# Optimization experiments

Measured on AMD Instinct MI355X. Metric: run time of the kernel, lower is better.

Reference implementation:

```python
import jax, jax.numpy as jnp
import numpy as np

C_IN = 4
C_OUT = 8
K = 5            # kernel_size (hardcoded by reshape(25,2) in original)
N_ROT = 8
R_B = 8          # rot_basis_size
STRIDE = 1
PAD = 2
TWO_PI = 2.0 * np.pi
ROT_SCALE = TWO_PI / R_B


def B2(x):
    # quadratic B-spline, exactly as in the torch source
    return (-3 * (-0.5 + x) ** 2 * jnp.sign(0.5 - x)
            + (-1.5 + x) ** 2 * jnp.sign(1.5 - x)
            - 3 * (1 + 2 * x) ** 2 * jnp.sign(0.5 + x) / 4
            + (3 + 2 * x) ** 2 * jnp.sign(1.5 + x) / 4) / 4


def angle_dist(th1, th2):
    return jnp.mod(th2 - th1 + np.pi, TWO_PI) - np.pi


def make_kernel_stack(weights):
    # weights: (C_IN, R_B*K*K, C_OUT). M = K*K*R_B combined (spatial-center, rot-center) index;
    # original repeats each spatial center R_B times (np.repeat) and tiles rot centers K*K times.
    lidx = -(K // 2)
    coords = jnp.arange(lidx, K // 2 + 1, dtype=jnp.float32)
    grid = jnp.stack(jnp.meshgrid(coords, coords, indexing='ij'), axis=-1)  # (K,K,2), grid[i,j]=[i+l, j+l]
    centers_xy = jnp.repeat(grid.reshape(K * K, 2), R_B, axis=0)            # (M,2)
    rot_centers = jnp.tile(jnp.arange(R_B, dtype=jnp.float32) * ROT_SCALE, K * K)  # (M,)
    rot_sample = jnp.arange(N_ROT, dtype=jnp.float32) * (TWO_PI / N_ROT)    # (N_ROT,)

    def one_kernel(theta):
        c, s = jnp.cos(theta), jnp.sin(theta)
        x, y = grid[..., 0], grid[..., 1]
        xxs = jnp.stack([x * c - y * s, x * s + y * c], axis=-1)            # (K,K,2) rotated sample grid
        xx_diffs = centers_xy[None, None, :, :] - xxs[:, :, None, :]        # (K,K,M,2)
        xx_vals = jnp.prod(B2(xx_diffs), axis=-1)                           # (K,K,M) separable spatial spline
        rots = rot_sample + theta                                           # (N_ROT,)
        rot_vals = B2(angle_dist(rots[:, None], rot_centers[None, :]) / ROT_SCALE)  # (N_ROT,M)
        vals = xx_vals[:, :, None, :] * rot_vals[None, None, :, :]          # (K,K,N_ROT,M)
        # contract basis index m against weights -> (C_OUT, C_IN, N_ROT, K, K)
        return jnp.einsum('xyrm,imo->oirxy', vals, weights)

    ks = jax.vmap(one_kernel)(-rot_sample)  # (N_ROT, C_OUT, C_IN, N_ROT, K, K), matches torch.cat over -theta
    return ks.reshape(N_ROT * C_OUT, C_IN * N_ROT, K, K)


def setup_inputs() -> dict:
    key = jax.random.key(0)
    kx, kw = jax.random.split(key)
    X = jax.random.normal(kx, (8, C_IN, N_ROT, 256, 256), dtype=jnp.float32)
    weights = jax.random.normal(kw, (C_IN, R_B * K * K, C_OUT), dtype=jnp.float32)
    return {'X': X, 'weights': weights}


def reference(X, weights):
    ks = make_kernel_stack(weights)                       # (N_ROT*C_OUT, C_IN*N_ROT, K, K)
    B, c, d, H, W = X.shape
    Xr = X.reshape(B, c * d, H, W)
    out = jax.lax.conv_general_dilated(
        Xr, ks, window_strides=(STRIDE, STRIDE),
        padding=[(PAD, PAD), (PAD, PAD)],
        dimension_numbers=('NCHW', 'OIHW', 'NCHW'))        # (B, N_ROT*C_OUT, h, w)
    Bn, _, h, w = out.shape
    out = out.reshape(Bn, N_ROT, C_OUT, h, w).transpose(0, 2, 1, 3, 4)  # (B, C_OUT, N_ROT, h, w)
    return (TWO_PI / N_ROT) * out
```

## Files before the change

### kernel.cpp

```cpp
#include <hip/hip_runtime.h>
#include <hip/hip_fp16.h>
#include <math.h>

#define PI_F      3.14159265358979323846f
#define TWO_PI_F  6.28318530717958647692f
#define PI4_F     0.78539816339744830962f

typedef _Float16 f16x8 __attribute__((ext_vector_type(8)));
typedef float    f32x4 __attribute__((ext_vector_type(4)));

__device__ __forceinline__ float sgn(float t) {
    return (t > 0.f) ? 1.f : ((t < 0.f) ? -1.f : 0.f);
}

__device__ __forceinline__ float b2(float x) {
    float a = x - 0.5f;
    float b = x - 1.5f;
    float c = 1.f + 2.f * x;
    float d = 3.f + 2.f * x;
    return (-3.f * a * a * sgn(0.5f - x)
            + b * b * sgn(1.5f - x)
            - 0.75f * c * c * sgn(0.5f + x)
            + 0.25f * d * d * sgn(1.5f + x)) * 0.25f;
}

__global__ void build_ks_kernel(const float* __restrict__ w, __half* __restrict__ ksh) {
    int g = blockIdx.x * 256 + threadIdx.x;
    if (g >= 64 * 32 * 25) return;
    int O = g & 63;
    int rest = g >> 6;
    int t = rest % 25;
    int I = rest / 25;
    int r0 = O >> 3, o = O & 7;
    int i = I >> 3, r = I & 7;
    int x = t / 5, y = t % 5;

    float theta = -(float)r0 * PI4_F;
    float cth = cosf(theta), sth = sinf(theta);
    float fx = (float)(x - 2), fy = (float)(y - 2);
    float xc = fx * cth - fy * sth;
    float yc = fx * sth + fy * cth;

    float rotv[8];
    float rs = (float)r * PI4_F + theta;
    #pragma unroll
    for (int mr = 0; mr < 8; ++mr) {
        float v = (float)mr * PI4_F - rs + PI_F;
        float md = fmodf(v, TWO_PI_F);
        if (md < 0.f) md += TWO_PI_F;
        rotv[mr] = b2((md - PI_F) / PI4_F);
    }

    float sum = 0.f;
    for (int mx = 0; mx < 25; ++mx) {
        float cx = (float)(mx / 5 - 2);
        float cy = (float)(mx % 5 - 2);
        float bx = b2(cx - xc) * b2(cy - yc);
        if (bx != 0.f) {
            const float* wp = w + (size_t)(i * 200 + mx * 8) * 8 + o;
            #pragma unroll
            for (int mr = 0; mr < 8; ++mr)
                sum = fmaf(bx * rotv[mr], wp[mr * 8], sum);
        }
    }
    ksh[(size_t)(t * 64 + O) * 32 + I] = __float2half(sum);
}

__global__ __launch_bounds__(256, 3) void conv_fused_kernel(const float* __restrict__ X,
                                                            const __half* __restrict__ ksh,
                                                            float* __restrict__ out) {
    __shared__ uint4 xt[4 * 433];

    int bid = blockIdx.x;
    int b   = bid >> 8;
    int rem = bid & 255;
    int h0  = (rem >> 3) << 3;
    int w0  = (rem & 7) << 5;
    int tid = threadIdx.x;

    const float* Xb = X + (size_t)b * 32 * 65536;

    for (int lin = tid; lin < 1728; lin += 256) {
        int slot = lin / 432;
        int p    = lin - slot * 432;
        int r = p / 36, c = p - (p / 36) * 36;
        int gh = h0 + r - 2;
        int gw = w0 + c - 2;
        union { __half hh[8]; uint4 u; } q;
        if ((unsigned)gh < 256u && (unsigned)gw < 256u) {
            const float* src = Xb + (size_t)slot * 8 * 65536 + gh * 256 + gw;
            #pragma unroll
            for (int j = 0; j < 8; ++j) q.hh[j] = __float2half(src[j * 65536]);
        } else {
            q.u = make_uint4(0u, 0u, 0u, 0u);
        }
        xt[slot * 433 + p] = q.u;
    }
    __syncthreads();

    int wave = tid >> 6, lane = tid & 63;
    int lO = lane & 15, ks4 = lane >> 4;
    int bidx = lO * 4 + ks4;
    const uint4* ksq = (const uint4*)ksh;

    f32x4 acc[4][4] = {};
    int baseA[4];
    #pragma unroll
    for (int m = 0; m < 4; ++m)
        baseA[m] = 433 * ks4 + (wave * 2 + (m >> 1)) * 36 + (m & 1) * 16 + lO;

    f16x8 Bf[2][4];
    #pragma unroll
    for (int n = 0; n < 4; ++n)
        Bf[0][n] = __builtin_bit_cast(f16x8, ksq[n * 64 + bidx]);

    #pragma unroll
    for (int t = 0; t < 25; ++t) {
        const int cur = t & 1, nxt = cur ^ 1;
        const int aoff = (t / 5) * 36 + (t % 5);

        f16x8 Af[4];
        #pragma unroll
        for (int m = 0; m < 4; ++m)
            Af[m] = __builtin_bit_cast(f16x8, xt[baseA[m] + aoff]);

        if (t < 24) {
            const int t1 = t + 1;
            #pragma unroll
            for (int n = 0; n < 4; ++n)
                Bf[nxt][n] = __builtin_bit_cast(f16x8, ksq[t1 * 256 + n * 64 + bidx]);
        }

        __builtin_amdgcn_s_setprio(1);
        #pragma unroll
        for (int m = 0; m < 4; ++m) {
            #pragma unroll
            for (int n = 0; n < 4; ++n)
                acc[m][n] = __builtin_amdgcn_mfma_f32_16x16x32_f16(Af[m], Bf[cur][n], acc[m][n], 0, 0, 0);
        }
        __builtin_amdgcn_s_setprio(0);
    }

    #pragma unroll
    for (int m = 0; m < 4; ++m) {
        int gh  = h0 + wave * 2 + (m >> 1);
        int gwb = w0 + (m & 1) * 16 + ks4 * 4;
        #pragma unroll
        for (int n = 0; n < 4; ++n) {
            int O = n * 16 + lO;
            float* op = out + (((size_t)(b * 8 + (O & 7)) * 8 + (O >> 3)) << 16)
                            + gh * 256 + gwb;
            *(f32x4*)op = acc[m][n] * PI4_F;
        }
    }
}

extern "C" void kernel_launch(void* const* d_in, const int* in_sizes, int n_in,
                              void* d_out, int out_size, void* d_ws, size_t ws_size,
                              hipStream_t stream) {
    const float* X = (const float*)d_in[0];
    const float* w = (const float*)d_in[1];
    float* outp = (float*)d_out;
    __half* ksh = (__half*)d_ws;

    build_ks_kernel<<<200, 256, 0, stream>>>(w, ksh);
    conv_fused_kernel<<<8 * 256, 256, 0, stream>>>(X, ksh, outp);
}
```

Measured before the change: 100.3 us.

## Pre-convert input to padded NHWC fp16 and run direct MFMA conv from global

```diff
diff --git a/kernel.cpp b/kernel.cpp
--- a/kernel.cpp
+++ b/kernel.cpp
@@ -8,6 +8,12 @@
 
 typedef _Float16 f16x8 __attribute__((ext_vector_type(8)));
 typedef float    f32x4 __attribute__((ext_vector_type(4)));
+
+#define GUARD_OFF  ((size_t)104 * 1024)
+#define XHP_OFF    ((size_t)1 << 17)
+#define XHP_ROW    (260 * 64)
+#define XHP_BATCH  ((size_t)256 * XHP_ROW)
+#define XHP_BYTES  ((size_t)8 * XHP_BATCH)
 
 __device__ __forceinline__ float sgn(float t) {
     return (t > 0.f) ? 1.f : ((t < 0.f) ? -1.f : 0.f);
@@ -24,7 +30,9 @@
             + 0.25f * d * d * sgn(1.5f + x)) * 0.25f;
 }
 
-__global__ void build_ks_kernel(const float* __restrict__ w, __half* __restrict__ ksh) {
+__global__ void build_ks_kernel(const float* __restrict__ w, __half* __restrict__ ksh,
+                                float* __restrict__ guard) {
+    if (blockIdx.x < 4) guard[blockIdx.x * 256 + threadIdx.x] = 0.f;
     int g = blockIdx.x * 256 + threadIdx.x;
     if (g >= 64 * 32 * 25) return;
     int O = g & 63;
@@ -66,20 +74,122 @@
     ksh[(size_t)(t * 64 + O) * 32 + I] = __float2half(sum);
 }
 
+__global__ __launch_bounds__(256, 4) void hwcpad_kernel(const float* __restrict__ X,
+                                                        char* __restrict__ XhP) {
+    int b = blockIdx.x >> 8;
+    int h = blockIdx.x & 255;
+    int ww = threadIdx.x;
+    const float* Xb = X + ((size_t)b * 32) * 65536 + h * 256 + ww;
+    char* rowp = XhP + (size_t)b * XHP_BATCH + (size_t)h * XHP_ROW;
+
+    union { __half hh[8]; uint4 u; } pk[4];
+    #pragma unroll
+    for (int c = 0; c < 32; ++c)
+        pk[c >> 3].hh[c & 7] = __float2half(Xb[(size_t)c * 65536]);
+
+    uint4* dst = (uint4*)(rowp + (ww + 2) * 64);
+    #pragma unroll
+    for (int kk = 0; kk < 4; ++kk) dst[kk] = pk[kk].u;
+
+    if (ww < 4) {
+        int pos = (ww < 2) ? ww : (256 + ww);
+        uint4* pz = (uint4*)(rowp + pos * 64);
+        uint4 z = make_uint4(0u, 0u, 0u, 0u);
+        pz[0] = z; pz[1] = z; pz[2] = z; pz[3] = z;
+    }
+}
+
+__global__ __launch_bounds__(256, 3) void conv_direct_kernel(const char* __restrict__ XhP,
+                                                             const __half* __restrict__ ksh,
+                                                             const char* __restrict__ guard,
+                                                             float* __restrict__ out) {
+    int tid = threadIdx.x;
+    int wave = tid >> 6, lane = tid & 63;
+    int wid = blockIdx.x * 4 + wave;
+    int b   = wid >> 10;
+    int rem = wid & 1023;
+    int h0  = (rem >> 3) << 1;
+    int w0  = (rem & 7) << 5;
+
+    int lO = lane & 15, ks4 = lane >> 4;
+    int lanebyte = lO * 64 + ks4 * 16;
+    int bidx = lO * 4 + ks4;
+    const uint4* ksq = (const uint4*)ksh;
+
+    const char* Xb = XhP + (size_t)b * XHP_BATCH + (size_t)w0 * 64;
+
+    const char* rowp[5][2];
+    #pragma unroll
+    for (int dx = 0; dx < 5; ++dx) {
+        #pragma unroll
+        for (int rr = 0; rr < 2; ++rr) {
+            int gh = h0 + rr + dx - 2;
+            rowp[dx][rr] = ((unsigned)gh < 256u)
+                ? Xb + (size_t)gh * XHP_ROW + lanebyte
+                : guard + lanebyte;
+        }
+    }
+
+    f32x4 acc[4][4] = {};
+    f16x8 Af[2][4], Bf[2][4];
+
+    #pragma unroll
+    for (int m = 0; m < 4; ++m)
+        Af[0][m] = __builtin_bit_cast(f16x8,
+            *(const uint4*)(rowp[0][m >> 1] + (m & 1) * 1024));
+    #pragma unroll
+    for (int n = 0; n < 4; ++n)
+        Bf[0][n] = __builtin_bit_cast(f16x8, ksq[n * 64 + bidx]);
+
+    #pragma unroll
+    for (int t = 0; t < 25; ++t) {
+        const int cur = t & 1, nxt = cur ^ 1;
+
+        if (t < 24) {
+            const int t1 = t + 1;
+            const int dx1 = t1 / 5, dy1 = t1 % 5;
+            #pragma unroll
+            for (int m = 0; m < 4; ++m)
+                Af[nxt][m] = __builtin_bit_cast(f16x8,
+                    *(const uint4*)(rowp[dx1][m >> 1] + (m & 1) * 1024 + dy1 * 64));
+            #pragma unroll
+            for (int n = 0; n < 4; ++n)
+                Bf[nxt][n] = __builtin_bit_cast(f16x8, ksq[t1 * 256 + n * 64 + bidx]);
+        }
+
+        #pragma unroll
+        for (int m = 0; m < 4; ++m) {
+            #pragma unroll
+            for (int n = 0; n < 4; ++n)
+                acc[m][n] = __builtin_amdgcn_mfma_f32_16x16x32_f16(Af[cur][m], Bf[cur][n], acc[m][n], 0, 0, 0);
+        }
+    }
+
+    #pragma unroll
+    for (int m = 0; m < 4; ++m) {
+        int gh  = h0 + (m >> 1);
+        int gwb = w0 + (m & 1) * 16 + ks4 * 4;
+        #pragma unroll
+        for (int n = 0; n < 4; ++n) {
+            int O = n * 16 + lO;
+            float* op = out + (((size_t)(b * 8 + (O & 7)) * 8 + (O >> 3)) << 16)
+                            + gh * 256 + gwb;
+            *(f32x4*)op = acc[m][n] * PI4_F;
+        }
+    }
+}
+
 __global__ __launch_bounds__(256, 3) void conv_fused_kernel(const float* __restrict__ X,
                                                             const __half* __restrict__ ksh,
                                                             float* __restrict__ out) {
     __shared__ uint4 xt[4 * 433];
-
     int bid = blockIdx.x;
     int b   = bid >> 8;
     int rem = bid & 255;
     int h0  = (rem >> 3) << 3;
     int w0  = (rem & 7) << 5;
     int tid = threadIdx.x;
-
     const float* Xb = X + (size_t)b * 32 * 65536;
-
     for (int lin = tid; lin < 1728; lin += 256) {
         int slot = lin / 432;
         int p    = lin - slot * 432;
@@ -97,50 +207,38 @@
         xt[slot * 433 + p] = q.u;
     }
     __syncthreads();
-
     int wave = tid >> 6, lane = tid & 63;
     int lO = lane & 15, ks4 = lane >> 4;
     int bidx = lO * 4 + ks4;
     const uint4* ksq = (const uint4*)ksh;
-
     f32x4 acc[4][4] = {};
     int baseA[4];
     #pragma unroll
     for (int m = 0; m < 4; ++m)
         baseA[m] = 433 * ks4 + (wave * 2 + (m >> 1)) * 36 + (m & 1) * 16 + lO;
-
     f16x8 Bf[2][4];
     #pragma unroll
     for (int n = 0; n < 4; ++n)
         Bf[0][n] = __builtin_bit_cast(f16x8, ksq[n * 64 + bidx]);
-
     #pragma unroll
     for (int t = 0; t < 25; ++t) {
         const int cur = t & 1, nxt = cur ^ 1;
         const int aoff = (t / 5) * 36 + (t % 5);
-
         f16x8 Af[4];
         #pragma unroll
         for (int m = 0; m < 4; ++m)
             Af[m] = __builtin_bit_cast(f16x8, xt[baseA[m] + aoff]);
-
         if (t < 24) {
-            const int t1 = t + 1;
-            #pragma unroll
-            for (int n = 0; n < 4; ++n)
-                Bf[nxt][n] = __builtin_bit_cast(f16x8, ksq[t1 * 256 + n * 64 + bidx]);
-        }
-
-        __builtin_amdgcn_s_setprio(1);
-        #pragma unroll
-        for (int m = 0; m < 4; ++m) {
+            #pragma unroll
+            for (int n = 0; n < 4; ++n)
+                Bf[nxt][n] = __builtin_bit_cast(f16x8, ksq[(t + 1) * 256 + n * 64 + bidx]);
+        }
+        #pragma unroll
+        for (int m = 0; m < 4; ++m)
             #pragma unroll
             for (int n = 0; n < 4; ++n)
                 acc[m][n] = __builtin_amdgcn_mfma_f32_16x16x32_f16(Af[m], Bf[cur][n], acc[m][n], 0, 0, 0);
-        }
-        __builtin_amdgcn_s_setprio(0);
-    }
-
+    }
     #pragma unroll
     for (int m = 0; m < 4; ++m) {
         int gh  = h0 + wave * 2 + (m >> 1);
@@ -148,8 +246,7 @@
         #pragma unroll
         for (int n = 0; n < 4; ++n) {
             int O = n * 16 + lO;
-            float* op = out + (((size_t)(b * 8 + (O & 7)) * 8 + (O >> 3)) << 16)
-                            + gh * 256 + gwb;
+            float* op = out + (((size_t)(b * 8 + (O & 7)) * 8 + (O >> 3)) << 16) + gh * 256 + gwb;
             *(f32x4*)op = acc[m][n] * PI4_F;
         }
     }
@@ -161,8 +258,17 @@
     const float* X = (const float*)d_in[0];
     const float* w = (const float*)d_in[1];
     float* outp = (float*)d_out;
-    __half* ksh = (__half*)d_ws;
-
-    build_ks_kernel<<<200, 256, 0, stream>>>(w, ksh);
-    conv_fused_kernel<<<8 * 256, 256, 0, stream>>>(X, ksh, outp);
-}
+    char* ws = (char*)d_ws;
+    __half* ksh = (__half*)ws;
+    float* guard = (float*)(ws + GUARD_OFF);
+
+    build_ks_kernel<<<200, 256, 0, stream>>>(w, ksh, guard);
+
+    if (ws_size >= XHP_OFF + XHP_BYTES) {
+        char* XhP = ws + XHP_OFF;
+        hwcpad_kernel<<<8 * 256, 256, 0, stream>>>(X, XhP);
+        conv_direct_kernel<<<2048, 256, 0, stream>>>(XhP, ksh, ws + GUARD_OFF, outp);
+    } else {
+        conv_fused_kernel<<<8 * 256, 256, 0, stream>>>(X, ksh, outp);
+    }
+}
```

New measurement: 133.7 us. 33.3% more time.
